# Optimization experiments

Measured on AMD Instinct MI355X. Metric: run time of the kernel, lower is better.

The kernel has to match this reference:

```python
import jax, jax.numpy as jnp
import numpy as np

EPS = 1e-06


def setup_inputs() -> dict:
    key = jax.random.key(0)
    ks = jax.random.split(key, 8)
    B, N, D, r, T, O, Hid = 32, 2048, 64, 32, 31, 12, 128
    in_dim = r + T  # 63
    xav = lambda k, shape: jax.random.uniform(k, shape, jnp.float32, -1.0, 1.0) * np.sqrt(6.0 / (shape[0] + shape[1]))
    return {
        "H": jax.random.normal(ks[0], (B, N, D), jnp.float32),
        "ts_out": jax.random.uniform(ks[1], (B, O, T), jnp.float32),
        "O": O,
        "P_raw": xav(ks[2], (N, r)),
        "Q_raw": xav(ks[3], (N, r)),
        "W1": xav(ks[4], (in_dim, Hid)),
        "b1": jnp.zeros((Hid,), jnp.float32),
        "W2": xav(ks[5], (Hid, r)),
        "b2": jnp.zeros((r,), jnp.float32),
        "alpha": jax.random.uniform(ks[6], (1,), jnp.float32),
    }


def reference(H, ts_out, O, P_raw, Q_raw, W1, b1, W2, b2, alpha):
    # nonnegative_basis=True -> softplus on both bases
    P = jax.nn.softplus(P_raw)  # [N, r]
    Q = jax.nn.softplus(Q_raw)  # [N, r]
    # Right contraction: U = Q^T H per batch -> [B, r, D]
    U = jnp.einsum('bnd,nr->brd', H, Q)
    # Context norm over feature dim: [B, r]
    ctx = jnp.sqrt(jnp.mean(U * U, axis=-1) + EPS)
    # Gate features: concat([ts_out [B,O,T], ctx broadcast to [B,O,r]])
    B = H.shape[0]
    ctx_exp = jnp.broadcast_to(ctx[:, None, :], (B, O, ctx.shape[-1]))
    feat = jnp.concatenate([ts_out, ctx_exp], axis=-1)  # [B, O, T+r]
    # scale MLP with exact (erf) GELU, dropout=0 (eval)
    h = jax.nn.gelu(feat @ W1 + b1, approximate=False)
    s = jax.nn.softplus(h @ W2 + b2)  # [B, O, r]
    # M = P (s \odot U) without materializing NxN: [B, O, N, D]
    M = jnp.einsum('bor,brd,nr->bond', s, U, P)
    a = jnp.clip(alpha[0], 0.0, 1.0)
    H_base = H[:, None, :, :]  # broadcast over O
    H_graph = H_base + a * (M - H_base)
    return H_graph
```

## Files before the change

kernel.cpp:

```cpp
#include <hip/hip_runtime.h>
#include <math.h>

#define B_ 32
#define N_ 2048
#define D_ 64
#define R_ 32
#define T_ 31
#define O_ 12
#define HID_ 128
#define IN_DIM_ 63
#define NCH_ 32

#define OFF_QSP   0
#define OFF_UPART (OFF_QSP + N_*R_)
#define OFF_U     (OFF_UPART + B_*NCH_*R_*D_)
#define OFF_CTX   (OFF_U + B_*R_*D_)
#define OFF_PBF   (OFF_CTX + B_*R_)
#define OFF_SUT   (OFF_PBF + N_*R_/2)

typedef __attribute__((ext_vector_type(4))) float f32x4;
typedef __attribute__((ext_vector_type(8))) short short8;

__device__ __forceinline__ float softplus_f(float x) {
    return fmaxf(x, 0.0f) + log1pf(expf(-fabsf(x)));
}
__device__ __forceinline__ float gelu_f(float x) {
    return 0.5f * x * (1.0f + erff(x * 0.70710678118654752440f));
}
__device__ __forceinline__ unsigned short f2bf(float f) {
    unsigned int u = __float_as_uint(f);
    u = (u + 0x7FFFu + ((u >> 16) & 1u)) >> 16;
    return (unsigned short)u;
}

__global__ __launch_bounds__(256) void k_softplus(const float* __restrict__ Qr,
                                                  float* __restrict__ ws) {
    int i = blockIdx.x * blockDim.x + threadIdx.x;
    if (i < N_ * R_) ws[OFF_QSP + i] = softplus_f(Qr[i]);
}

__global__ __launch_bounds__(512) void k_upart(const float* __restrict__ H,
                                               const float* __restrict__ Pr,
                                               float* __restrict__ ws) {
    const float* __restrict__ Qsp = ws + OFF_QSP;
    float* __restrict__ Upart = ws + OFF_UPART;
    int b = blockIdx.x / NCH_;
    int c = blockIdx.x % NCH_;
    int tid = threadIdx.x;
    const int n0 = c * (N_ / NCH_);

    if (b == 0) {
        unsigned short* Pbf = (unsigned short*)(ws + OFF_PBF);
        #pragma unroll
        for (int i = tid; i < 64 * R_; i += 512)
            Pbf[(size_t)n0 * R_ + i] = f2bf(softplus_f(Pr[(size_t)n0 * R_ + i]));
    }

    int d = tid & 63;
    int rb = __builtin_amdgcn_readfirstlane(tid >> 6);
    const int r0 = rb * 4;
    float acc0 = 0.f, acc1 = 0.f, acc2 = 0.f, acc3 = 0.f;
    const float* __restrict__ Hb = H + ((size_t)b * N_ + n0) * D_ + d;
    #pragma unroll 2
    for (int i = 0; i < 64; ++i) {
        int n = n0 + i;
        float h = Hb[(size_t)i * D_];
        const float* q = Qsp + (size_t)n * R_ + r0;
        acc0 = fmaf(h, q[0], acc0);
        acc1 = fmaf(h, q[1], acc1);
        acc2 = fmaf(h, q[2], acc2);
        acc3 = fmaf(h, q[3], acc3);
    }
    float* up = Upart + ((size_t)(b * NCH_ + c) * R_ + r0) * D_ + d;
    up[0 * D_] = acc0;
    up[1 * D_] = acc1;
    up[2 * D_] = acc2;
    up[3 * D_] = acc3;
}

__global__ __launch_bounds__(256) void k_ured(float* __restrict__ ws) {
    const float* __restrict__ Upart = ws + OFF_UPART;
    float* __restrict__ U = ws + OFF_U;
    float* __restrict__ ctx = ws + OFF_CTX;
    int b = blockIdx.x;
    int r = blockIdx.y * 4 + (threadIdx.x >> 6);
    int d = threadIdx.x & 63;
    float u = 0.f;
    #pragma unroll 8
    for (int c = 0; c < NCH_; ++c)
        u += Upart[((size_t)(b * NCH_ + c) * R_ + r) * D_ + d];
    U[((size_t)b * R_ + r) * D_ + d] = u;
    float sq = u * u;
    #pragma unroll
    for (int off = 32; off; off >>= 1) sq += __shfl_xor(sq, off, 64);
    if (d == 0) ctx[b * R_ + r] = sqrtf(sq * (1.0f / D_) + 1e-6f);
}

__global__ __launch_bounds__(128) void k_mlp(const float* __restrict__ ts_out,
                                             const float* __restrict__ W1,
                                             const float* __restrict__ b1,
                                             const float* __restrict__ W2,
                                             const float* __restrict__ b2,
                                             const float* __restrict__ alpha,
                                             float* __restrict__ ws) {
    __shared__ float feat[IN_DIM_];
    __shared__ float hsh[HID_];
    __shared__ float ssh[R_];
    int bo = blockIdx.x;
    int b = bo / O_;
    int tid = threadIdx.x;
    const float* __restrict__ ctx = ws + OFF_CTX;
    if (tid < T_) feat[tid] = ts_out[(size_t)bo * T_ + tid];
    else if (tid < IN_DIM_) feat[tid] = ctx[b * R_ + (tid - T_)];
    __syncthreads();
    float acc = b1[tid];
    #pragma unroll 9
    for (int k = 0; k < IN_DIM_; ++k) acc = fmaf(feat[k], W1[k * HID_ + tid], acc);
    hsh[tid] = gelu_f(acc);
    __syncthreads();
    if (tid < R_) {
        float a2 = b2[tid];
        #pragma unroll 8
        for (int j = 0; j < HID_; ++j) a2 = fmaf(hsh[j], W2[j * R_ + tid], a2);
        ssh[tid] = softplus_f(a2);
    }
    __syncthreads();
    float a = fminf(fmaxf(alpha[0], 0.0f), 1.0f);
    const float* __restrict__ U = ws + OFF_U;
    unsigned short* SUT = (unsigned short*)(ws + OFF_SUT) + (size_t)bo * D_ * R_;
    #pragma unroll
    for (int idx = tid; idx < D_ * R_; idx += 128) {
        int d = idx >> 5, r = idx & 31;
        SUT[idx] = f2bf(a * ssh[r] * U[((size_t)b * R_ + r) * D_ + d]);
    }
}

__global__ __launch_bounds__(256) void k_main(const float* __restrict__ H,
                                              const float* __restrict__ alpha,
                                              const float* __restrict__ ws,
                                              float* __restrict__ out) {
    __shared__ float tile[64 * 64];
    const int b = blockIdx.z;
    const int og = blockIdx.y;
    const int nblk = blockIdx.x * 64;
    const int tid = threadIdx.x;
    const int w = tid >> 6;
    const int lane = tid & 63;
    const int l16 = lane & 15;
    const int lhi = lane >> 4;
    const int rl = w * 16 + l16;
    const float a = fminf(fmaxf(alpha[0], 0.0f), 1.0f);
    const float oma = 1.0f - a;

    const unsigned short* Pbf = (const unsigned short*)(ws + OFF_PBF);
    const unsigned short* SUT0 = (const unsigned short*)(ws + OFF_SUT)
                               + (size_t)(b * O_ + og * 6) * D_ * R_;

    short8 pfrag = *(const short8*)(Pbf + (size_t)(nblk + rl) * R_ + lhi * 8);

    const float* __restrict__ Hrow = H + ((size_t)b * N_ + nblk + rl) * D_;
    f32x4 homa[4];
    #pragma unroll
    for (int db = 0; db < 4; ++db)
        homa[db] = oma * *(const f32x4*)(Hrow + db * 16 + lhi * 4);

    char* tb = (char*)tile;
    float* __restrict__ oblk = out + ((size_t)(b * O_ + og * 6) * N_ + nblk) * D_;

    short8 sf[2][4];
    #pragma unroll
    for (int db = 0; db < 4; ++db)
        sf[0][db] = *(const short8*)(SUT0 + (size_t)(db * 16 + l16) * R_ + lhi * 8);
    #pragma unroll
    for (int oi = 0; oi < 6; ++oi) {
        const int cur = oi & 1, nxt = cur ^ 1;
        if (oi < 5) {
            const unsigned short* Sn = SUT0 + (size_t)(oi + 1) * D_ * R_;
            #pragma unroll
            for (int db = 0; db < 4; ++db)
                sf[nxt][db] = *(const short8*)(Sn + (size_t)(db * 16 + l16) * R_ + lhi * 8);
        }
        #pragma unroll
        for (int db = 0; db < 4; ++db) {
            f32x4 v = homa[db] + __builtin_amdgcn_mfma_f32_16x16x32_bf16(
                sf[cur][db], pfrag, (f32x4){0.f, 0.f, 0.f, 0.f}, 0, 0, 0);
            int c = (db * 64 + lhi * 16) ^ ((rl & 7) << 4);
            *(f32x4*)(tb + rl * 256 + c) = v;
        }
        char* op = (char*)(oblk + (size_t)oi * N_ * D_);
        #pragma unroll
        for (int i = 0; i < 4; ++i) {
            int g = w * 4096 + i * 1024 + lane * 16;
            int rr = g >> 8;
            int cc = (g & 255) ^ ((rr & 7) << 4);
            f32x4 v = *(const f32x4*)(tb + rr * 256 + cc);
            *(f32x4*)(op + g) = v;
        }
    }
}

extern "C" void kernel_launch(void* const* d_in, const int* in_sizes, int n_in,
                              void* d_out, int out_size, void* d_ws, size_t ws_size,
                              hipStream_t stream) {
    const float* H      = (const float*)d_in[0];
    const float* ts_out = (const float*)d_in[1];
    const float* P_raw  = (const float*)d_in[3];
    const float* Q_raw  = (const float*)d_in[4];
    const float* W1     = (const float*)d_in[5];
    const float* b1     = (const float*)d_in[6];
    const float* W2     = (const float*)d_in[7];
    const float* b2     = (const float*)d_in[8];
    const float* alpha  = (const float*)d_in[9];
    float* out = (float*)d_out;
    float* ws  = (float*)d_ws;

    k_softplus<<<dim3((N_ * R_ + 255) / 256), dim3(256), 0, stream>>>(Q_raw, ws);
    k_upart<<<dim3(B_ * NCH_), dim3(512), 0, stream>>>(H, P_raw, ws);
    k_ured<<<dim3(B_, 8), dim3(256), 0, stream>>>(ws);
    k_mlp<<<dim3(B_ * O_), dim3(128), 0, stream>>>(ts_out, W1, b1, W2, b2, alpha, ws);
    k_main<<<dim3(N_ / 64, 2, B_), dim3(256), 0, stream>>>(H, alpha, ws, out);
}
```

Baseline: 74.14 us.

## Fuse U reduction, ctx norm and MLP into one per-batch tail kernel

Merges the partial-U reduction, context norm, gate MLP and scaled-U bf16 packing into a single per-batch kernel that keeps U in shared memory, which removes one launch and the global U round trip. Cuts the N chunk count from 32 to 8, so k_upart runs fewer, longer blocks and leaves fewer partials to reduce. In k_main the grid is reordered so the two O-groups sharing an H tile are adjacent blocks, and SUT fragments are now prefetched two steps ahead with a triple buffer. The tail kernel now uses only 32 blocks, which may lower parallelism for the MLP work.

```diff
diff --git a/kernel.cpp b/kernel.cpp
--- a/kernel.cpp
+++ b/kernel.cpp
@@ -9,12 +9,11 @@
 #define O_ 12
 #define HID_ 128
 #define IN_DIM_ 63
-#define NCH_ 32
+#define NCH_ 8
 
 #define OFF_QSP   0
 #define OFF_UPART (OFF_QSP + N_*R_)
-#define OFF_U     (OFF_UPART + B_*NCH_*R_*D_)
-#define OFF_CTX   (OFF_U + B_*R_*D_)
+#define OFF_CTX   (OFF_UPART + B_*NCH_*R_*D_)
 #define OFF_PBF   (OFF_CTX + B_*R_)
 #define OFF_SUT   (OFF_PBF + N_*R_/2)
 
@@ -52,7 +51,7 @@
     if (b == 0) {
         unsigned short* Pbf = (unsigned short*)(ws + OFF_PBF);
         #pragma unroll
-        for (int i = tid; i < 64 * R_; i += 512)
+        for (int i = tid; i < (N_ / NCH_) * R_; i += 512)
             Pbf[(size_t)n0 * R_ + i] = f2bf(softplus_f(Pr[(size_t)n0 * R_ + i]));
     }
 
@@ -62,10 +61,9 @@
     float acc0 = 0.f, acc1 = 0.f, acc2 = 0.f, acc3 = 0.f;
     const float* __restrict__ Hb = H + ((size_t)b * N_ + n0) * D_ + d;
     #pragma unroll 2
-    for (int i = 0; i < 64; ++i) {
-        int n = n0 + i;
+    for (int i = 0; i < N_ / NCH_; ++i) {
         float h = Hb[(size_t)i * D_];
-        const float* q = Qsp + (size_t)n * R_ + r0;
+        const float* q = Qsp + (size_t)(n0 + i) * R_ + r0;
         acc0 = fmaf(h, q[0], acc0);
         acc1 = fmaf(h, q[1], acc1);
         acc2 = fmaf(h, q[2], acc2);
@@ -78,60 +76,70 @@
     up[3 * D_] = acc3;
 }
 
-__global__ __launch_bounds__(256) void k_ured(float* __restrict__ ws) {
+__global__ __launch_bounds__(256) void k_tail(const float* __restrict__ ts_out,
+                                              const float* __restrict__ W1,
+                                              const float* __restrict__ b1,
+                                              const float* __restrict__ W2,
+                                              const float* __restrict__ b2,
+                                              const float* __restrict__ alpha,
+                                              float* __restrict__ ws) {
+    __shared__ float Ul[R_][D_];
+    __shared__ float ctxl[R_];
+    __shared__ float tsl[O_ * T_];
+    __shared__ float hsh[O_][HID_];
+    __shared__ float ssh[O_][R_];
+    int b = blockIdx.x;
+    int tid = threadIdx.x;
     const float* __restrict__ Upart = ws + OFF_UPART;
-    float* __restrict__ U = ws + OFF_U;
-    float* __restrict__ ctx = ws + OFF_CTX;
-    int b = blockIdx.x;
-    int r = blockIdx.y * 4 + (threadIdx.x >> 6);
-    int d = threadIdx.x & 63;
-    float u = 0.f;
-    #pragma unroll 8
-    for (int c = 0; c < NCH_; ++c)
-        u += Upart[((size_t)(b * NCH_ + c) * R_ + r) * D_ + d];
-    U[((size_t)b * R_ + r) * D_ + d] = u;
-    float sq = u * u;
-    #pragma unroll
-    for (int off = 32; off; off >>= 1) sq += __shfl_xor(sq, off, 64);
-    if (d == 0) ctx[b * R_ + r] = sqrtf(sq * (1.0f / D_) + 1e-6f);
-}
-
-__global__ __launch_bounds__(128) void k_mlp(const float* __restrict__ ts_out,
-                                             const float* __restrict__ W1,
-                                             const float* __restrict__ b1,
-                                             const float* __restrict__ W2,
-                                             const float* __restrict__ b2,
-                                             const float* __restrict__ alpha,
-                                             float* __restrict__ ws) {
-    __shared__ float feat[IN_DIM_];
-    __shared__ float hsh[HID_];
-    __shared__ float ssh[R_];
-    int bo = blockIdx.x;
-    int b = bo / O_;
-    int tid = threadIdx.x;
-    const float* __restrict__ ctx = ws + OFF_CTX;
-    if (tid < T_) feat[tid] = ts_out[(size_t)bo * T_ + tid];
-    else if (tid < IN_DIM_) feat[tid] = ctx[b * R_ + (tid - T_)];
+
+    {
+        int r = tid >> 3;
+        int d0 = (tid & 7) * 8;
+        f32x4 u0 = {0.f,0.f,0.f,0.f}, u1 = {0.f,0.f,0.f,0.f};
+        #pragma unroll
+        for (int c = 0; c < NCH_; ++c) {
+            const float* p = Upart + ((size_t)(b * NCH_ + c) * R_ + r) * D_ + d0;
+            u0 += *(const f32x4*)(p);
+            u1 += *(const f32x4*)(p + 4);
+        }
+        *(f32x4*)(&Ul[r][d0])     = u0;
+        *(f32x4*)(&Ul[r][d0 + 4]) = u1;
+        float sq = u0[0]*u0[0]+u0[1]*u0[1]+u0[2]*u0[2]+u0[3]*u0[3]
+                 + u1[0]*u1[0]+u1[1]*u1[1]+u1[2]*u1[2]+u1[3]*u1[3];
+        #pragma unroll
+        for (int off = 4; off; off >>= 1) sq += __shfl_xor(sq, off, 8);
+        if ((tid & 7) == 0) ctxl[r] = sqrtf(sq * (1.0f / D_) + 1e-6f);
+    }
+    for (int i = tid; i < O_ * T_; i += 256)
+        tsl[i] = ts_out[(size_t)b * O_ * T_ + i];
     __syncthreads();
-    float acc = b1[tid];
-    #pragma unroll 9
-    for (int k = 0; k < IN_DIM_; ++k) acc = fmaf(feat[k], W1[k * HID_ + tid], acc);
-    hsh[tid] = gelu_f(acc);
+
+    int g = tid >> 7;
+    int lt = tid & 127;
+    #pragma unroll
+    for (int oo = 0; oo < 6; ++oo) {
+        int o = g + oo * 2;
+        float acc = b1[lt];
+        for (int k = 0; k < T_; ++k) acc = fmaf(tsl[o * T_ + k], W1[k * HID_ + lt], acc);
+        for (int k = 0; k < R_; ++k) acc = fmaf(ctxl[k], W1[(T_ + k) * HID_ + lt], acc);
+        hsh[o][lt] = gelu_f(acc);
+    }
     __syncthreads();
-    if (tid < R_) {
-        float a2 = b2[tid];
+    if (tid < O_ * R_ - 128) {  }
+    for (int idx = tid; idx < O_ * R_; idx += 256) {
+        int o = idx >> 5, r = idx & 31;
+        float a2 = b2[r];
         #pragma unroll 8
-        for (int j = 0; j < HID_; ++j) a2 = fmaf(hsh[j], W2[j * R_ + tid], a2);
-        ssh[tid] = softplus_f(a2);
+        for (int j = 0; j < HID_; ++j) a2 = fmaf(hsh[o][j], W2[j * R_ + r], a2);
+        ssh[o][r] = softplus_f(a2);
     }
     __syncthreads();
+
     float a = fminf(fmaxf(alpha[0], 0.0f), 1.0f);
-    const float* __restrict__ U = ws + OFF_U;
-    unsigned short* SUT = (unsigned short*)(ws + OFF_SUT) + (size_t)bo * D_ * R_;
-    #pragma unroll
-    for (int idx = tid; idx < D_ * R_; idx += 128) {
-        int d = idx >> 5, r = idx & 31;
-        SUT[idx] = f2bf(a * ssh[r] * U[((size_t)b * R_ + r) * D_ + d]);
+    unsigned short* SUT = (unsigned short*)(ws + OFF_SUT) + (size_t)b * O_ * D_ * R_;
+    for (int idx = tid; idx < O_ * D_ * R_; idx += 256) {
+        int r = idx & 31, d = (idx >> 5) & 63, o = idx >> 11;
+        SUT[idx] = f2bf(a * ssh[o][r] * Ul[r][d]);
     }
 }
 
@@ -140,9 +148,9 @@
                                               const float* __restrict__ ws,
                                               float* __restrict__ out) {
     __shared__ float tile[64 * 64];
+    const int og = blockIdx.x;
     const int b = blockIdx.z;
-    const int og = blockIdx.y;
-    const int nblk = blockIdx.x * 64;
+    const int nblk = blockIdx.y * 64;
     const int tid = threadIdx.x;
     const int w = tid >> 6;
     const int lane = tid & 63;
@@ -156,29 +164,34 @@
     const unsigned short* SUT0 = (const unsigned short*)(ws + OFF_SUT)
                                + (size_t)(b * O_ + og * 6) * D_ * R_;
 
+    const float* __restrict__ Hrow = H + ((size_t)b * N_ + nblk + rl) * D_;
+    f32x4 hv[4];
+    #pragma unroll
+    for (int db = 0; db < 4; ++db)
+        hv[db] = *(const f32x4*)(Hrow + db * 16 + lhi * 4);
     short8 pfrag = *(const short8*)(Pbf + (size_t)(nblk + rl) * R_ + lhi * 8);
-
-    const float* __restrict__ Hrow = H + ((size_t)b * N_ + nblk + rl) * D_;
+    short8 sf[3][4];
+    #pragma unroll
+    for (int db = 0; db < 4; ++db) {
+        sf[0][db] = *(const short8*)(SUT0 + (size_t)(db * 16 + l16) * R_ + lhi * 8);
+        sf[1][db] = *(const short8*)(SUT0 + (size_t)(D_ * R_ + (db * 16 + l16) * R_) + lhi * 8);
+    }
     f32x4 homa[4];
     #pragma unroll
-    for (int db = 0; db < 4; ++db)
-        homa[db] = oma * *(const f32x4*)(Hrow + db * 16 + lhi * 4);
+    for (int db = 0; db < 4; ++db) homa[db] = oma * hv[db];
 
     char* tb = (char*)tile;
     float* __restrict__ oblk = out + ((size_t)(b * O_ + og * 6) * N_ + nblk) * D_;
 
-    short8 sf[2][4];
-    #pragma unroll
-    for (int db = 0; db < 4; ++db)
-        sf[0][db] = *(const short8*)(SUT0 + (size_t)(db * 16 + l16) * R_ + lhi * 8);
     #pragma unroll
     for (int oi = 0; oi < 6; ++oi) {
-        const int cur = oi & 1, nxt = cur ^ 1;
-        if (oi < 5) {
-            const unsigned short* Sn = SUT0 + (size_t)(oi + 1) * D_ * R_;
+        const int cur = oi % 3;
+        if (oi < 4) {
+            const int nx2 = (oi + 2) % 3;
+            const unsigned short* Sn = SUT0 + (size_t)(oi + 2) * D_ * R_;
             #pragma unroll
             for (int db = 0; db < 4; ++db)
-                sf[nxt][db] = *(const short8*)(Sn + (size_t)(db * 16 + l16) * R_ + lhi * 8);
+                sf[nx2][db] = *(const short8*)(Sn + (size_t)(db * 16 + l16) * R_ + lhi * 8);
         }
         #pragma unroll
         for (int db = 0; db < 4; ++db) {
@@ -190,11 +203,11 @@
         char* op = (char*)(oblk + (size_t)oi * N_ * D_);
         #pragma unroll
         for (int i = 0; i < 4; ++i) {
-            int g = w * 4096 + i * 1024 + lane * 16;
-            int rr = g >> 8;
-            int cc = (g & 255) ^ ((rr & 7) << 4);
+            int gg = w * 4096 + i * 1024 + lane * 16;
+            int rr = gg >> 8;
+            int cc = (gg & 255) ^ ((rr & 7) << 4);
             f32x4 v = *(const f32x4*)(tb + rr * 256 + cc);
-            *(f32x4*)(op + g) = v;
+            *(f32x4*)(op + gg) = v;
         }
     }
 }
@@ -216,7 +229,6 @@
 
     k_softplus<<<dim3((N_ * R_ + 255) / 256), dim3(256), 0, stream>>>(Q_raw, ws);
     k_upart<<<dim3(B_ * NCH_), dim3(512), 0, stream>>>(H, P_raw, ws);
-    k_ured<<<dim3(B_, 8), dim3(256), 0, stream>>>(ws);
-    k_mlp<<<dim3(B_ * O_), dim3(128), 0, stream>>>(ts_out, W1, b1, W2, b2, alpha, ws);
-    k_main<<<dim3(N_ / 64, 2, B_), dim3(256), 0, stream>>>(H, alpha, ws, out);
-}
+    k_tail<<<dim3(B_), dim3(256), 0, stream>>>(ts_out, W1, b1, W2, b2, alpha, ws);
+    k_main<<<dim3(2, N_ / 64, B_), dim3(256), 0, stream>>>(H, alpha, ws, out);
+}
```

Measured after the change: 114.6 us. 1.55x slower.
